# Kernel tuning notes

Measured on AMD Instinct MI355X. Metric: run time of the kernel, lower is better.

The kernel has to match this reference:

```python
import jax, jax.numpy as jnp
import numpy as np

D_MODEL = 1024
N_HEADS = 16
D_K = 64
D_FF = 4096
B = 8
S = 1024
NEG = -1e32
EPS = 1e-5


def _layer_norm(x, g, b):
    mu = jnp.mean(x, axis=-1, keepdims=True)
    var = jnp.var(x, axis=-1, keepdims=True)
    return (x - mu) * jax.lax.rsqrt(var + EPS) * g + b


def setup_inputs() -> dict:
    key = jax.random.key(0)
    ks = jax.random.split(key, 16)
    sc = 0.02
    inp = {
        'x': jax.random.normal(ks[0], (B, S, D_MODEL), dtype=jnp.float32),
        'Wq': jax.random.normal(ks[1], (D_MODEL, D_MODEL), jnp.float32) * sc,
        'bq': jnp.zeros((D_MODEL,), jnp.float32),
        'Wk': jax.random.normal(ks[2], (D_MODEL, D_MODEL), jnp.float32) * sc,
        'bk': jnp.zeros((D_MODEL,), jnp.float32),
        'Wv': jax.random.normal(ks[3], (D_MODEL, D_MODEL), jnp.float32) * sc,
        'bv': jnp.zeros((D_MODEL,), jnp.float32),
        'Wo': jax.random.normal(ks[4], (D_MODEL, D_MODEL), jnp.float32) * sc,
        'bo': jnp.zeros((D_MODEL,), jnp.float32),
        'W1': jax.random.normal(ks[5], (D_MODEL, D_FF), jnp.float32) * sc,
        'b1': jnp.zeros((D_FF,), jnp.float32),
        'W2': jax.random.normal(ks[6], (D_FF, D_MODEL), jnp.float32) * sc,
        'b2': jnp.zeros((D_MODEL,), jnp.float32),
        'g1': jnp.ones((D_MODEL,), jnp.float32),
        'beta1': jnp.zeros((D_MODEL,), jnp.float32),
        'g3': jnp.ones((D_MODEL,), jnp.float32),
        'beta3': jnp.zeros((D_MODEL,), jnp.float32),
    }
    return inp


def _block(x, Wq, bq, Wk, bk, Wv, bv, Wo, bo, W1, b1, W2, b2, g1, beta1, g3, beta3):
    bs, seqlen, _ = x.shape
    # QKV projections -> [b, h, s, d_k]
    def split_heads(t):
        return t.reshape(bs, seqlen, N_HEADS, D_K).transpose(0, 2, 1, 3)
    q = split_heads(x @ Wq + bq)
    k = split_heads(x @ Wk + bk)
    v = split_heads(x @ Wv + bv)
    # scores [b,h,s,s]
    scores = jnp.einsum('bhqd,bhkd->bhqk', q, k) / jnp.sqrt(jnp.float32(D_K))
    # mask=0 case: src_mask = (triu(ones, k=0) == 0) -> allow strictly lower (j < i)
    i = jnp.arange(seqlen)[:, None]
    j = jnp.arange(seqlen)[None, :]
    allowed = (j < i)  # [s, s]
    scores = jnp.where(allowed[None, None], scores, NEG)
    attn = jax.nn.softmax(scores, axis=-1)
    # zero_pad: zero out the first query row of attention probs
    attn = attn * (i > 0).astype(attn.dtype)[None, None]
    ctx = jnp.einsum('bhqk,bhkd->bhqd', attn, v)  # [b,h,s,d_k]
    concat = ctx.transpose(0, 2, 1, 3).reshape(bs, seqlen, D_MODEL)
    attn_out = concat @ Wo + bo
    # residual + LN (dropout p=0)
    h1 = _layer_norm(x + attn_out, g1, beta1)
    # position-wise FFN
    ffn = jax.nn.relu(h1 @ W1 + b1) @ W2 + b2
    out = _layer_norm(h1 + ffn, g3, beta3)
    return out


def reference(x, Wq, bq, Wk, bk, Wv, bv, Wo, bo, W1, b1, W2, b2, g1, beta1, g3, beta3):
    return _block(x, Wq, bq, Wk, bk, Wv, bv, Wo, bo, W1, b1, W2, b2, g1, beta1, g3, beta3)
```

## Files before the change

### kernel.cpp

```cpp
#include <hip/hip_runtime.h>
#include <hip/hip_bf16.h>

typedef __bf16 bf16x8 __attribute__((ext_vector_type(8)));
typedef __bf16 bf16x4 __attribute__((ext_vector_type(4)));
typedef float f32x4 __attribute__((ext_vector_type(4)));
typedef float f32x16 __attribute__((ext_vector_type(16)));

#define GLOBAL_LOAD_LDS16(gp, lp)                                              \
  __builtin_amdgcn_global_load_lds(                                            \
      (const __attribute__((address_space(1))) void*)(gp),                     \
      (__attribute__((address_space(3))) void*)(lp), 16, 0, 0)

__global__ __launch_bounds__(256) void transpose4_f2b_k(
    const float* __restrict__ s0, const float* __restrict__ s1,
    const float* __restrict__ s2, const float* __restrict__ s3,
    __bf16* __restrict__ dst) {
  __shared__ float tile[32][33];
  const float* srcs[4] = {s0, s1, s2, s3};
  const float* src = srcs[blockIdx.z];
  __bf16* d = dst + ((size_t)blockIdx.z << 20);
  const int bx = blockIdx.x * 32, by = blockIdx.y * 32;
  const int tx = threadIdx.x & 31, ty = threadIdx.x >> 5;
#pragma unroll
  for (int i = 0; i < 32; i += 8)
    tile[ty + i][tx] = src[(size_t)(by + ty + i) * 1024 + bx + tx];
  __syncthreads();
#pragma unroll
  for (int i = 0; i < 32; i += 8)
    d[(size_t)(bx + ty + i) * 1024 + by + tx] = (__bf16)tile[tx][ty + i];
}

__global__ __launch_bounds__(256) void transpose_f2b_k(
    const float* __restrict__ src, __bf16* __restrict__ dst, int R, int C) {
  __shared__ float tile[32][33];
  const int bx = blockIdx.x * 32, by = blockIdx.y * 32;
  const int tx = threadIdx.x & 31, ty = threadIdx.x >> 5;
#pragma unroll
  for (int i = 0; i < 32; i += 8)
    tile[ty + i][tx] = src[(size_t)(by + ty + i) * C + bx + tx];
  __syncthreads();
#pragma unroll
  for (int i = 0; i < 32; i += 8)
    dst[(size_t)(bx + ty + i) * R + by + tx] = (__bf16)tile[tx][ty + i];
}

__global__ __launch_bounds__(256) void transpose_v_k(
    const __bf16* __restrict__ src, __bf16* __restrict__ dst) {
  __shared__ __bf16 tile[32][33];
  const int bh = blockIdx.z;
  const int s0 = blockIdx.x * 32, d0 = blockIdx.y * 32;
  const size_t base = (size_t)bh << 16;
  const int tx = threadIdx.x & 31, ty = threadIdx.x >> 5;
#pragma unroll
  for (int i = 0; i < 32; i += 8)
    tile[ty + i][tx] = src[base + (size_t)(s0 + ty + i) * 64 + d0 + tx];
  __syncthreads();
#pragma unroll
  for (int i = 0; i < 32; i += 8)
    dst[base + (size_t)(d0 + ty + i) * 1024 + s0 + tx] = tile[tx][ty + i];
}

__global__ __launch_bounds__(256) void convert_f2b_k(const float* __restrict__ s,
                                                     __bf16* __restrict__ d) {
  const size_t i = ((size_t)blockIdx.x * 256 + threadIdx.x) * 4;
  const float4 v = *(const float4*)(s + i);
  bf16x4 o;
  o[0] = (__bf16)v.x; o[1] = (__bf16)v.y; o[2] = (__bf16)v.z; o[3] = (__bf16)v.w;
  *(bf16x4*)(d + i) = o;
}

__global__ void concat3_k(const float* a, const float* b, const float* c,
                          float* o) {
  int i = blockIdx.x * 256 + threadIdx.x;
  if (i < 1024) o[i] = a[i];
  else if (i < 2048) o[i] = b[i - 1024];
  else if (i < 3072) o[i] = c[i - 2048];
}

template <int EPI>
__global__ __launch_bounds__(256) void gemm_bt32(const __bf16* __restrict__ A,
                                                 const __bf16* __restrict__ Bt,
                                                 const float* __restrict__ bias,
                                                 __bf16* __restrict__ C,
                                                 int M, int N, int K) {
  __shared__ __align__(16) __bf16 As[128 * 64];
  __shared__ __align__(16) __bf16 Bs[128 * 64];
  const int tid = threadIdx.x;
  const int wave = tid >> 6, lane = tid & 63;
  const int l31 = lane & 31, hi = lane >> 5;
  const int wm = wave >> 1, wn = wave & 1;
  const int m0 = blockIdx.x * 128, n0 = blockIdx.y * 128;
  const int srsub = lane >> 3;
  const int sch = lane & 7;

  f32x16 acc[2][2] = {};

  for (int k0 = 0; k0 < K; k0 += 64) {
#pragma unroll
    for (int p = 0; p < 4; ++p) {
      const int g = wave * 4 + p;
      const int row = g * 8 + srsub;
      GLOBAL_LOAD_LDS16(A + (size_t)(m0 + row) * K + k0 + ((sch ^ (row & 7)) * 8),
                        As + g * 512);
      GLOBAL_LOAD_LDS16(Bt + (size_t)(n0 + row) * K + k0 + ((sch ^ (row & 7)) * 8),
                        Bs + g * 512);
    }
    __syncthreads();
#pragma unroll
    for (int kk = 0; kk < 4; ++kk) {
      bf16x8 af[2], bf[2];
#pragma unroll
      for (int mt = 0; mt < 2; ++mt) {
        const int row = wm * 64 + mt * 32 + l31;
        af[mt] = *(const bf16x8*)(As + row * 64 +
                                  (((kk * 2 + hi) ^ (row & 7)) * 8));
      }
#pragma unroll
      for (int nt = 0; nt < 2; ++nt) {
        const int row = wn * 64 + nt * 32 + l31;
        bf[nt] = *(const bf16x8*)(Bs + row * 64 +
                                  (((kk * 2 + hi) ^ (row & 7)) * 8));
      }
#pragma unroll
      for (int mt = 0; mt < 2; ++mt)
#pragma unroll
        for (int nt = 0; nt < 2; ++nt)
          acc[mt][nt] = __builtin_amdgcn_mfma_f32_32x32x16_bf16(
              af[mt], bf[nt], acc[mt][nt], 0, 0, 0);
    }
    __syncthreads();
  }

  float bvv[2];
#pragma unroll
  for (int nt = 0; nt < 2; ++nt) bvv[nt] = bias[n0 + wn * 64 + nt * 32 + l31];
#pragma unroll
  for (int mt = 0; mt < 2; ++mt) {
#pragma unroll
    for (int i = 0; i < 16; ++i) {
      const int row = m0 + wm * 64 + mt * 32 + (i & 3) + 8 * (i >> 2) + 4 * hi;
#pragma unroll
      for (int nt = 0; nt < 2; ++nt) {
        const int col = n0 + wn * 64 + nt * 32 + l31;
        float v = acc[mt][nt][i] + bvv[nt];
        if (EPI == 1) v = fmaxf(v, 0.0f);
        size_t oidx;
        if (EPI == 2) {
          const int which = col >> 10, wi = col & 1023;
          const int h = wi >> 6, d = wi & 63;
          const int b = row >> 10, s = row & 1023;
          oidx = ((size_t)which << 23) +
                 (((size_t)(b * 16 + h) << 16) + s * 64 + d);
        } else {
          oidx = (size_t)row * N + col;
        }
        C[oidx] = (__bf16)v;
      }
    }
  }
}

__global__ __launch_bounds__(256) void gemm_bt64(const __bf16* __restrict__ A,
                                                 const __bf16* __restrict__ Bt,
                                                 const float* __restrict__ bias,
                                                 __bf16* __restrict__ C,
                                                 int M, int N, int K) {
  __shared__ __align__(16) __bf16 As[128 * 64];
  __shared__ __align__(16) __bf16 Bs[64 * 64];
  const int tid = threadIdx.x;
  const int wave = tid >> 6, lane = tid & 63;
  const int quad = lane >> 4, l15 = lane & 15;
  const int wm = wave >> 1, wn = wave & 1;
  const int m0 = blockIdx.x * 128, n0 = blockIdx.y * 64;
  const int srow = tid >> 3;
  const int sch = tid & 7;

  f32x4 acc[4][2] = {};

  for (int k0 = 0; k0 < K; k0 += 64) {
#pragma unroll
    for (int p = 0; p < 4; ++p) {
      const int row = p * 32 + srow;
      GLOBAL_LOAD_LDS16(A + (size_t)(m0 + row) * K + k0 + ((sch ^ (row & 7)) * 8),
                        As + p * 2048 + wave * 512);
    }
#pragma unroll
    for (int p = 0; p < 2; ++p) {
      const int row = p * 32 + srow;
      GLOBAL_LOAD_LDS16(Bt + (size_t)(n0 + row) * K + k0 + ((sch ^ (row & 7)) * 8),
                        Bs + p * 2048 + wave * 512);
    }
    __syncthreads();
    bf16x8 af[4][2], bfr[2][2];
#pragma unroll
    for (int kk = 0; kk < 2; ++kk) {
#pragma unroll
      for (int mt = 0; mt < 4; ++mt) {
        const int row = wm * 64 + mt * 16 + l15;
        af[mt][kk] =
            *(const bf16x8*)(As + row * 64 + (((kk * 4 + quad) ^ (row & 7)) * 8));
      }
#pragma unroll
      for (int nt = 0; nt < 2; ++nt) {
        const int row = wn * 32 + nt * 16 + l15;
        bfr[nt][kk] =
            *(const bf16x8*)(Bs + row * 64 + (((kk * 4 + quad) ^ (row & 7)) * 8));
      }
    }
#pragma unroll
    for (int kk = 0; kk < 2; ++kk)
#pragma unroll
      for (int mt = 0; mt < 4; ++mt)
#pragma unroll
        for (int nt = 0; nt < 2; ++nt)
          acc[mt][nt] = __builtin_amdgcn_mfma_f32_16x16x32_bf16(
              af[mt][kk], bfr[nt][kk], acc[mt][nt], 0, 0, 0);
    __syncthreads();
  }

  float bv[2];
#pragma unroll
  for (int nt = 0; nt < 2; ++nt) bv[nt] = bias[n0 + wn * 32 + nt * 16 + l15];
#pragma unroll
  for (int mt = 0; mt < 4; ++mt) {
#pragma unroll
    for (int r = 0; r < 4; ++r) {
      const int row = m0 + wm * 64 + mt * 16 + quad * 4 + r;
#pragma unroll
      for (int nt = 0; nt < 2; ++nt) {
        const int col = n0 + wn * 32 + nt * 16 + l15;
        C[(size_t)row * N + col] = (__bf16)(acc[mt][nt][r] + bv[nt]);
      }
    }
  }
}

__global__ __launch_bounds__(256) void attn_kernel(const __bf16* __restrict__ Q,
                                                   const __bf16* __restrict__ Kg,
                                                   const __bf16* __restrict__ Vt,
                                                   __bf16* __restrict__ ctx) {
  const int qp = blockIdx.x;
  const int bh = blockIdx.y;
  const int b = bh >> 4, h = bh & 15;
  const int tid = threadIdx.x, wave = tid >> 6, lane = tid & 63;
  const int quad = lane >> 4, l15 = lane & 15;
  const size_t hoff = (size_t)bh << 16;
  const __bf16* Qh = Q + hoff;
  const __bf16* Kh = Kg + hoff;
  const __bf16* Vh = Vt + hoff;

  __shared__ __align__(16) __bf16 Ks[64 * 64];
  __shared__ __align__(16) __bf16 Vs[64 * 64];
  __shared__ __align__(16) __bf16 Ps[4][32 * 72];
  __shared__ float lL[128];

  const int skey = wave * 8 + (lane >> 3);
  const int sgr = lane & 7;

#pragma unroll
  for (int pass = 0; pass < 2; ++pass) {
    const int qt = pass ? (7 - qp) : qp;
    const int qb = qt * 128;

    bf16x8 qf[2][2];
#pragma unroll
    for (int g = 0; g < 2; ++g) {
      const int qrow = qb + wave * 32 + g * 16 + l15;
      bf16x8 t0 = *(const bf16x8*)(Qh + (size_t)qrow * 64 + quad * 8);
      bf16x8 t1 = *(const bf16x8*)(Qh + (size_t)qrow * 64 + 32 + quad * 8);
#pragma unroll
      for (int e = 0; e < 8; ++e) {
        qf[g][0][e] = (__bf16)((float)t0[e] * 0.125f);
        qf[g][1][e] = (__bf16)((float)t1[e] * 0.125f);
      }
    }

    f32x4 oacc[4][2] = {};
    float lrun[2][4] = {};

    const int ktmax = 2 * qt + 1;
    for (int kt = 0; kt <= ktmax; ++kt) {
      __syncthreads();
#pragma unroll
      for (int j = 0; j < 2; ++j) {
        const int row = skey + 32 * j;
        GLOBAL_LOAD_LDS16(
            Kh + (size_t)(kt * 64 + row) * 64 + ((sgr ^ (row & 7)) * 8),
            Ks + j * 2048 + wave * 512);
        GLOBAL_LOAD_LDS16(
            Vh + (size_t)row * 1024 + kt * 64 + ((sgr ^ (row & 7)) * 8),
            Vs + j * 2048 + wave * 512);
      }
      __syncthreads();

      f32x4 sacc[2][4] = {};
#pragma unroll
      for (int nt = 0; nt < 4; ++nt) {
        const int key = nt * 16 + l15, sw = key & 7;
        bf16x8 kf0 = *(const bf16x8*)(Ks + key * 64 + ((quad ^ sw) * 8));
        bf16x8 kf1 = *(const bf16x8*)(Ks + key * 64 + (((quad + 4) ^ sw) * 8));
#pragma unroll
        for (int g = 0; g < 2; ++g) {
          sacc[g][nt] = __builtin_amdgcn_mfma_f32_16x16x32_bf16(
              qf[g][0], kf0, sacc[g][nt], 0, 0, 0);
          sacc[g][nt] = __builtin_amdgcn_mfma_f32_16x16x32_bf16(
              qf[g][1], kf1, sacc[g][nt], 0, 0, 0);
        }
      }

      const bool tilemask = (kt >= 2 * qt);
#pragma unroll
      for (int g = 0; g < 2; ++g)
#pragma unroll
        for (int nt = 0; nt < 4; ++nt) {
          const int key = kt * 64 + nt * 16 + l15;
#pragma unroll
          for (int r = 0; r < 4; ++r) {
            float p = __expf(fminf(sacc[g][nt][r], 60.0f));
            if (tilemask && key >= qb + wave * 32 + g * 16 + quad * 4 + r)
              p = 0.0f;
            sacc[g][nt][r] = p;
            lrun[g][r] += p;
          }
        }

#pragma unroll
      for (int g = 0; g < 2; ++g)
#pragma unroll
        for (int nt = 0; nt < 4; ++nt)
#pragma unroll
          for (int r = 0; r < 4; ++r)
            Ps[wave][(g * 16 + quad * 4 + r) * 72 + nt * 16 + l15] =
                (__bf16)sacc[g][nt][r];

#pragma unroll
      for (int kc = 0; kc < 2; ++kc) {
        bf16x8 pf[2];
#pragma unroll
        for (int g = 0; g < 2; ++g)
          pf[g] = *(const bf16x8*)(&Ps[wave][(g * 16 + l15) * 72 + kc * 32 +
                                             quad * 8]);
#pragma unroll
        for (int mdt = 0; mdt < 4; ++mdt) {
          const int d = mdt * 16 + l15, sw = d & 7;
          bf16x8 vf =
              *(const bf16x8*)(Vs + d * 64 + (((kc * 4 + quad) ^ sw) * 8));
#pragma unroll
          for (int g = 0; g < 2; ++g)
            oacc[mdt][g] = __builtin_amdgcn_mfma_f32_16x16x32_bf16(
                vf, pf[g], oacc[mdt][g], 0, 0, 0);
        }
      }
    }

#pragma unroll
    for (int g = 0; g < 2; ++g)
#pragma unroll
      for (int r = 0; r < 4; ++r) {
        float s = lrun[g][r];
#pragma unroll
        for (int d = 1; d < 16; d <<= 1) s += __shfl_xor(s, d);
        if (l15 == 0) lL[wave * 32 + g * 16 + quad * 4 + r] = s;
      }
    float linv[2];
#pragma unroll
    for (int g = 0; g < 2; ++g) {
      const float l = lL[wave * 32 + g * 16 + l15];
      linv[g] = (qb + wave * 32 + g * 16 + l15 == 0) ? 0.0f : (1.0f / l);
    }
    __bf16* Ot = Ps[wave];
#pragma unroll
    for (int mdt = 0; mdt < 4; ++mdt)
#pragma unroll
      for (int g = 0; g < 2; ++g)
#pragma unroll
        for (int r = 0; r < 4; ++r)
          Ot[(g * 16 + l15) * 72 + mdt * 16 + quad * 4 + r] =
              (__bf16)(oacc[mdt][g][r] * linv[g]);
#pragma unroll
    for (int rr = 0; rr < 2; ++rr)
#pragma unroll
      for (int j = 0; j < 2; ++j) {
        const int row = rr * 16 + (lane >> 2), chk = (lane & 3) + 4 * j;
        bf16x8 ov = *(const bf16x8*)(Ot + row * 72 + chk * 8);
        const size_t oi = ((size_t)(b * 1024 + qb + wave * 32 + row)) * 1024 +
                          h * 64 + chk * 8;
        *(bf16x8*)(ctx + oi) = ov;
      }
  }
}

template <typename TX, typename TY, typename TO>
__global__ __launch_bounds__(256) void add_ln_kernel(const TX* __restrict__ x,
                                                     const TY* __restrict__ y,
                                                     const float* __restrict__ g,
                                                     const float* __restrict__ be,
                                                     TO* __restrict__ out) {
  const int row = blockIdx.x;
  const size_t base = (size_t)row * 1024;
  const int t = threadIdx.x;
  float xv[4], yv[4];
  if constexpr (sizeof(TX) == 4) {
    const float4 a = *(const float4*)(x + base + t * 4);
    xv[0] = a.x; xv[1] = a.y; xv[2] = a.z; xv[3] = a.w;
  } else {
    const bf16x4 a = *(const bf16x4*)(x + base + t * 4);
#pragma unroll
    for (int i = 0; i < 4; ++i) xv[i] = (float)a[i];
  }
  if constexpr (sizeof(TY) == 4) {
    const float4 a = *(const float4*)(y + base + t * 4);
    yv[0] = a.x; yv[1] = a.y; yv[2] = a.z; yv[3] = a.w;
  } else {
    const bf16x4 a = *(const bf16x4*)(y + base + t * 4);
#pragma unroll
    for (int i = 0; i < 4; ++i) yv[i] = (float)a[i];
  }
  float v[4], s = 0.0f, s2 = 0.0f;
#pragma unroll
  for (int i = 0; i < 4; ++i) {
    v[i] = xv[i] + yv[i];
    s += v[i];
    s2 += v[i] * v[i];
  }
#pragma unroll
  for (int m = 1; m < 64; m <<= 1) {
    s += __shfl_xor(s, m);
    s2 += __shfl_xor(s2, m);
  }
  __shared__ float ss[4], ss2[4];
  const int w = t >> 6;
  if ((t & 63) == 0) { ss[w] = s; ss2[w] = s2; }
  __syncthreads();
  s = ss[0] + ss[1] + ss[2] + ss[3];
  s2 = ss2[0] + ss2[1] + ss2[2] + ss2[3];
  const float mu = s * (1.0f / 1024.0f);
  const float var = s2 * (1.0f / 1024.0f) - mu * mu;
  const float rstd = rsqrtf(var + 1e-5f);
#pragma unroll
  for (int i = 0; i < 4; ++i) {
    const float o = (v[i] - mu) * rstd * g[t * 4 + i] + be[t * 4 + i];
    out[base + t * 4 + i] = (TO)o;
  }
}

extern "C" void kernel_launch(void* const* d_in, const int* in_sizes, int n_in,
                              void* d_out, int out_size, void* d_ws,
                              size_t ws_size, hipStream_t stream) {
  (void)in_sizes; (void)n_in; (void)out_size; (void)ws_size;
  const float* x   = (const float*)d_in[0];
  const float* Wq  = (const float*)d_in[1];
  const float* bq  = (const float*)d_in[2];
  const float* Wk  = (const float*)d_in[3];
  const float* bk  = (const float*)d_in[4];
  const float* Wv  = (const float*)d_in[5];
  const float* bv  = (const float*)d_in[6];
  const float* Wo  = (const float*)d_in[7];
  const float* bo  = (const float*)d_in[8];
  const float* W1  = (const float*)d_in[9];
  const float* b1  = (const float*)d_in[10];
  const float* W2  = (const float*)d_in[11];
  const float* b2  = (const float*)d_in[12];
  const float* g1  = (const float*)d_in[13];
  const float* be1 = (const float*)d_in[14];
  const float* g3  = (const float*)d_in[15];
  const float* be3 = (const float*)d_in[16];

  char* ws = (char*)d_ws;
  __bf16* Qb    = (__bf16*)(ws + 0);
  __bf16* Kb    = (__bf16*)(ws + (16u << 20));
  __bf16* Vb    = (__bf16*)(ws + (32u << 20));
  __bf16* ctx   = (__bf16*)(ws + (48u << 20));
  __bf16* mid   = (__bf16*)(ws + 0);
  __bf16* aout  = (__bf16*)(ws + (64u << 20));
  __bf16* h1    = aout;
  __bf16* xb    = (__bf16*)(ws + (80u << 20));
  __bf16* Vtb   = (__bf16*)(ws + (80u << 20));
  __bf16* fout  = (__bf16*)(ws + (80u << 20));
  __bf16* WqkvT = (__bf16*)(ws + (96u << 20));
  __bf16* WoT   = (__bf16*)(ws + (96u << 20) + 3 * (1u << 21));
  __bf16* W1T   = (__bf16*)(ws + (104u << 20));
  __bf16* W2T   = (__bf16*)(ws + (112u << 20));
  float*  bqkv  = (float*)(ws + (120u << 20));
  float*  outp  = (float*)d_out;

  const dim3 blk(256);
  convert_f2b_k<<<dim3(8192), blk, 0, stream>>>(x, xb);
  transpose4_f2b_k<<<dim3(32, 32, 4), blk, 0, stream>>>(Wq, Wk, Wv, Wo, WqkvT);
  transpose_f2b_k<<<dim3(128, 32), blk, 0, stream>>>(W1, W1T, 1024, 4096);
  transpose_f2b_k<<<dim3(32, 128), blk, 0, stream>>>(W2, W2T, 4096, 1024);
  concat3_k<<<dim3(12), blk, 0, stream>>>(bq, bk, bv, bqkv);

  gemm_bt32<2><<<dim3(64, 24), blk, 0, stream>>>(xb, WqkvT, bqkv, Qb, 8192, 3072, 1024);
  transpose_v_k<<<dim3(32, 2, 128), blk, 0, stream>>>(Vb, Vtb);
  attn_kernel<<<dim3(4, 128), blk, 0, stream>>>(Qb, Kb, Vtb, ctx);
  gemm_bt64<<<dim3(64, 16), blk, 0, stream>>>(ctx, WoT, bo, aout, 8192, 1024, 1024);
  add_ln_kernel<float, __bf16, __bf16><<<dim3(8192), blk, 0, stream>>>(
      x, aout, g1, be1, h1);
  gemm_bt32<1><<<dim3(64, 32), blk, 0, stream>>>(h1, W1T, b1, mid, 8192, 4096, 1024);
  gemm_bt64<<<dim3(64, 16), blk, 0, stream>>>(mid, W2T, b2, fout, 8192, 1024, 4096);
  add_ln_kernel<__bf16, __bf16, float><<<dim3(8192), blk, 0, stream>>>(
      h1, fout, g3, be3, outp);
}
```

Before: 482.5 us.

## Replace 128x128 GEMM with double-buffered 256x256 ping-pong GEMM for QKV and FFN1

Swaps the single-buffered 128x128 tile GEMM for a 512-thread, 256x256-tile kernel used by the QKV projection and the first FFN matmul. The new kernel double-buffers the LDS tiles and interleaves global-to-LDS loads with 16x16x32 MFMA phases, using barriers and s_setprio. It also remaps block IDs so that neighbouring tiles spread across the XCDs. The goal is to hide load latency behind compute and raise reuse per tile. The cost is 128KB of LDS per block and fragile hand-placed waitcnt and barrier scheduling.

```diff
diff --git a/kernel.cpp b/kernel.cpp
--- a/kernel.cpp
+++ b/kernel.cpp
@@ -77,87 +77,189 @@
   else if (i < 3072) o[i] = c[i - 2048];
 }
 
+#define STG(P, rowbase, Kld, kbase, DST)                                       \
+  do {                                                                         \
+    GLOBAL_LOAD_LDS16((P) + (size_t)((rowbase) + wave * 16 + srow) * (Kld) +   \
+                          (kbase) + sch8,                                      \
+                      (DST) + wave * 1024);                                    \
+    GLOBAL_LOAD_LDS16((P) + (size_t)((rowbase) + wave * 16 + 8 + srow) *       \
+                              (Kld) + (kbase) + sch8,                          \
+                      (DST) + wave * 1024 + 512);                              \
+  } while (0)
+
+#define LDA(BUF, HALF)                                                         \
+  do {                                                                         \
+    const __bf16* pA_ = &As[BUF][HALF][aoff];                                  \
+    _Pragma("unroll") for (int f_ = 0; f_ < 4; ++f_) {                         \
+      af[f_][0] = *(const bf16x8*)(pA_ + f_ * 1024 + c0);                      \
+      af[f_][1] = *(const bf16x8*)(pA_ + f_ * 1024 + (c0 ^ 32));               \
+    }                                                                          \
+  } while (0)
+
+#define LDB(BUF, CB)                                                           \
+  do {                                                                         \
+    const __bf16* pB_ = &Bs[BUF][CB][boff];                                    \
+    _Pragma("unroll") for (int g_ = 0; g_ < 2; ++g_) {                         \
+      bfr[CB][g_][0] = *(const bf16x8*)(pB_ + g_ * 1024 + c0);                 \
+      bfr[CB][g_][1] = *(const bf16x8*)(pB_ + g_ * 1024 + (c0 ^ 32));          \
+    }                                                                          \
+  } while (0)
+
+#define MFMA16(rb, cb)                                                         \
+  do {                                                                         \
+    _Pragma("unroll") for (int f_ = 0; f_ < 4; ++f_)                           \
+        _Pragma("unroll") for (int g_ = 0; g_ < 2; ++g_) {                     \
+      acc[rb][f_][cb][g_] = __builtin_amdgcn_mfma_f32_16x16x32_bf16(           \
+          af[f_][0], bfr[cb][g_][0], acc[rb][f_][cb][g_], 0, 0, 0);            \
+      acc[rb][f_][cb][g_] = __builtin_amdgcn_mfma_f32_16x16x32_bf16(           \
+          af[f_][1], bfr[cb][g_][1], acc[rb][f_][cb][g_], 0, 0, 0);            \
+    }                                                                          \
+  } while (0)
+
+#define PH_MID()                                                               \
+  do {                                                                         \
+    asm volatile("" ::: "memory");                                             \
+    __builtin_amdgcn_s_barrier();                                              \
+    asm volatile("s_waitcnt lgkmcnt(0)" ::: "memory");                         \
+    __builtin_amdgcn_s_setprio(1);                                             \
+  } while (0)
+
+#define PH_END()                                                               \
+  do {                                                                         \
+    __builtin_amdgcn_s_setprio(0);                                             \
+    asm volatile("" ::: "memory");                                             \
+    __builtin_amdgcn_s_barrier();                                              \
+    asm volatile("" ::: "memory");                                             \
+  } while (0)
+
+#define PH_END_VM(NVM)                                                         \
+  do {                                                                         \
+    __builtin_amdgcn_s_setprio(0);                                             \
+    asm volatile("s_waitcnt vmcnt(" #NVM ")" ::: "memory");                    \
+    __builtin_amdgcn_s_barrier();                                              \
+    asm volatile("" ::: "memory");                                             \
+  } while (0)
+
 template <int EPI>
-__global__ __launch_bounds__(256) void gemm_bt32(const __bf16* __restrict__ A,
-                                                 const __bf16* __restrict__ Bt,
-                                                 const float* __restrict__ bias,
-                                                 __bf16* __restrict__ C,
-                                                 int M, int N, int K) {
-  __shared__ __align__(16) __bf16 As[128 * 64];
-  __shared__ __align__(16) __bf16 Bs[128 * 64];
+__global__ __launch_bounds__(512, 2) void gemm256(const __bf16* __restrict__ A,
+                                                  const __bf16* __restrict__ Bt,
+                                                  const float* __restrict__ bias,
+                                                  __bf16* __restrict__ C,
+                                                  int M, int N, int K) {
+  __shared__ __align__(16) __bf16 As[2][2][128 * 64];
+  __shared__ __align__(16) __bf16 Bs[2][2][128 * 64];
   const int tid = threadIdx.x;
   const int wave = tid >> 6, lane = tid & 63;
-  const int l31 = lane & 31, hi = lane >> 5;
-  const int wm = wave >> 1, wn = wave & 1;
-  const int m0 = blockIdx.x * 128, n0 = blockIdx.y * 128;
-  const int srsub = lane >> 3;
-  const int sch = lane & 7;
-
-  f32x16 acc[2][2] = {};
-
-  for (int k0 = 0; k0 < K; k0 += 64) {
-#pragma unroll
-    for (int p = 0; p < 4; ++p) {
-      const int g = wave * 4 + p;
-      const int row = g * 8 + srsub;
-      GLOBAL_LOAD_LDS16(A + (size_t)(m0 + row) * K + k0 + ((sch ^ (row & 7)) * 8),
-                        As + g * 512);
-      GLOBAL_LOAD_LDS16(Bt + (size_t)(n0 + row) * K + k0 + ((sch ^ (row & 7)) * 8),
-                        Bs + g * 512);
-    }
-    __syncthreads();
-#pragma unroll
-    for (int kk = 0; kk < 4; ++kk) {
-      bf16x8 af[2], bf[2];
-#pragma unroll
-      for (int mt = 0; mt < 2; ++mt) {
-        const int row = wm * 64 + mt * 32 + l31;
-        af[mt] = *(const bf16x8*)(As + row * 64 +
-                                  (((kk * 2 + hi) ^ (row & 7)) * 8));
-      }
-#pragma unroll
-      for (int nt = 0; nt < 2; ++nt) {
-        const int row = wn * 64 + nt * 32 + l31;
-        bf[nt] = *(const bf16x8*)(Bs + row * 64 +
-                                  (((kk * 2 + hi) ^ (row & 7)) * 8));
-      }
-#pragma unroll
-      for (int mt = 0; mt < 2; ++mt)
-#pragma unroll
-        for (int nt = 0; nt < 2; ++nt)
-          acc[mt][nt] = __builtin_amdgcn_mfma_f32_32x32x16_bf16(
-              af[mt], bf[nt], acc[mt][nt], 0, 0, 0);
-    }
-    __syncthreads();
-  }
-
-  float bvv[2];
-#pragma unroll
-  for (int nt = 0; nt < 2; ++nt) bvv[nt] = bias[n0 + wn * 64 + nt * 32 + l31];
-#pragma unroll
-  for (int mt = 0; mt < 2; ++mt) {
-#pragma unroll
-    for (int i = 0; i < 16; ++i) {
-      const int row = m0 + wm * 64 + mt * 32 + (i & 3) + 8 * (i >> 2) + 4 * hi;
-#pragma unroll
-      for (int nt = 0; nt < 2; ++nt) {
-        const int col = n0 + wn * 64 + nt * 32 + l31;
-        float v = acc[mt][nt][i] + bvv[nt];
-        if (EPI == 1) v = fmaxf(v, 0.0f);
-        size_t oidx;
-        if (EPI == 2) {
-          const int which = col >> 10, wi = col & 1023;
-          const int h = wi >> 6, d = wi & 63;
-          const int b = row >> 10, s = row & 1023;
-          oidx = ((size_t)which << 23) +
-                 (((size_t)(b * 16 + h) << 16) + s * 64 + d);
-        } else {
-          oidx = (size_t)row * N + col;
-        }
-        C[oidx] = (__bf16)v;
-      }
-    }
-  }
+  const int quad = lane >> 4, l15 = lane & 15;
+  const int wm = wave >> 2, wn = wave & 3;
+
+  const int nwg = gridDim.x;
+  const int cpx = nwg >> 3;
+  const int bid = blockIdx.x;
+  const int wg = (bid & 7) * cpx + (bid >> 3);
+  const int gy = N >> 8;
+  const int tm = wg / gy, tn = wg - tm * gy;
+  const int m0 = tm << 8, n0 = tn << 8;
+
+  const int srow = lane >> 3;
+  const int sch8 = ((lane & 7) ^ srow) * 8;
+  const int aoff = (wm * 64 + l15) * 64;
+  const int boff = (wn * 32 + l15) * 64;
+  const int c0 = (quad ^ (l15 & 7)) * 8;
+
+  bf16x8 af[4][2], bfr[2][2][2];
+  f32x4 acc[2][4][2][2] = {};
+
+  const int NJ = K >> 7;
+
+  STG(A, m0, K, 0, &As[0][0][0]);
+  STG(Bt, n0, K, 0, &Bs[0][0][0]);
+  STG(A, m0 + 128, K, 0, &As[0][1][0]);
+  STG(Bt, n0 + 128, K, 0, &Bs[0][1][0]);
+  STG(A, m0, K, 64, &As[1][0][0]);
+  STG(Bt, n0, K, 64, &Bs[1][0][0]);
+  asm volatile("s_waitcnt vmcnt(4)" ::: "memory");
+  __builtin_amdgcn_s_barrier();
+  asm volatile("" ::: "memory");
+
+  for (int j = 0; j < NJ; ++j) {
+    const int t1k = (j << 7) + 64, t2k = (j << 7) + 128, t3k = (j << 7) + 192;
+    const bool pf = (j + 1 < NJ);
+    LDA(0, 0);
+    LDB(0, 0);
+    STG(A, m0 + 128, K, t1k, &As[1][1][0]);
+    PH_MID();
+    MFMA16(0, 0);
+    PH_END();
+    LDB(0, 1);
+    STG(Bt, n0 + 128, K, t1k, &Bs[1][1][0]);
+    PH_MID();
+    MFMA16(0, 1);
+    PH_END();
+    LDA(0, 1);
+    if (pf) STG(A, m0, K, t2k, &As[0][0][0]);
+    PH_MID();
+    MFMA16(1, 0);
+    PH_END();
+    if (pf) STG(Bt, n0, K, t2k, &Bs[0][0][0]);
+    PH_MID();
+    MFMA16(1, 1);
+    if (pf) PH_END_VM(4); else PH_END_VM(0);
+    LDA(1, 0);
+    LDB(1, 0);
+    if (pf) STG(A, m0 + 128, K, t2k, &As[0][1][0]);
+    PH_MID();
+    MFMA16(0, 0);
+    PH_END();
+    LDB(1, 1);
+    if (pf) STG(Bt, n0 + 128, K, t2k, &Bs[0][1][0]);
+    PH_MID();
+    MFMA16(0, 1);
+    PH_END();
+    LDA(1, 1);
+    if (pf) STG(A, m0, K, t3k, &As[1][0][0]);
+    PH_MID();
+    MFMA16(1, 0);
+    PH_END();
+    if (pf) STG(Bt, n0, K, t3k, &Bs[1][0][0]);
+    PH_MID();
+    MFMA16(1, 1);
+    if (pf) PH_END_VM(4); else PH_END();
+  }
+
+  float bvv[2][2];
+#pragma unroll
+  for (int cb = 0; cb < 2; ++cb)
+#pragma unroll
+    for (int g = 0; g < 2; ++g)
+      bvv[cb][g] = bias[n0 + cb * 128 + wn * 32 + g * 16 + l15];
+#pragma unroll
+  for (int rb = 0; rb < 2; ++rb)
+#pragma unroll
+    for (int f = 0; f < 4; ++f)
+#pragma unroll
+      for (int i = 0; i < 4; ++i) {
+        const int row = m0 + rb * 128 + wm * 64 + f * 16 + quad * 4 + i;
+#pragma unroll
+        for (int cb = 0; cb < 2; ++cb)
+#pragma unroll
+          for (int g = 0; g < 2; ++g) {
+            const int col = n0 + cb * 128 + wn * 32 + g * 16 + l15;
+            float v = acc[rb][f][cb][g][i] + bvv[cb][g];
+            if (EPI == 1) v = fmaxf(v, 0.0f);
+            size_t oidx;
+            if (EPI == 2) {
+              const int which = col >> 10, wi = col & 1023;
+              const int h = wi >> 6, d = wi & 63;
+              const int b = row >> 10, s = row & 1023;
+              oidx = ((size_t)which << 23) +
+                     (((size_t)(b * 16 + h) << 16) + s * 64 + d);
+            } else {
+              oidx = (size_t)row * N + col;
+            }
+            C[oidx] = (__bf16)v;
+          }
+      }
 }
 
 __global__ __launch_bounds__(256) void gemm_bt64(const __bf16* __restrict__ A,
@@ -485,19 +587,22 @@
   float*  outp  = (float*)d_out;
 
   const dim3 blk(256);
+  const dim3 blk512(512);
   convert_f2b_k<<<dim3(8192), blk, 0, stream>>>(x, xb);
   transpose4_f2b_k<<<dim3(32, 32, 4), blk, 0, stream>>>(Wq, Wk, Wv, Wo, WqkvT);
   transpose_f2b_k<<<dim3(128, 32), blk, 0, stream>>>(W1, W1T, 1024, 4096);
   transpose_f2b_k<<<dim3(32, 128), blk, 0, stream>>>(W2, W2T, 4096, 1024);
   concat3_k<<<dim3(12), blk, 0, stream>>>(bq, bk, bv, bqkv);
 
-  gemm_bt32<2><<<dim3(64, 24), blk, 0, stream>>>(xb, WqkvT, bqkv, Qb, 8192, 3072, 1024);
+  gemm256<2><<<dim3(32 * 12), blk512, 0, stream>>>(xb, WqkvT, bqkv, Qb,
+                                                   8192, 3072, 1024);
   transpose_v_k<<<dim3(32, 2, 128), blk, 0, stream>>>(Vb, Vtb);
   attn_kernel<<<dim3(4, 128), blk, 0, stream>>>(Qb, Kb, Vtb, ctx);
   gemm_bt64<<<dim3(64, 16), blk, 0, stream>>>(ctx, WoT, bo, aout, 8192, 1024, 1024);
   add_ln_kernel<float, __bf16, __bf16><<<dim3(8192), blk, 0, stream>>>(
       x, aout, g1, be1, h1);
-  gemm_bt32<1><<<dim3(64, 32), blk, 0, stream>>>(h1, W1T, b1, mid, 8192, 4096, 1024);
+  gemm256<1><<<dim3(32 * 16), blk512, 0, stream>>>(h1, W1T, b1, mid,
+                                                   8192, 4096, 1024);
   gemm_bt64<<<dim3(64, 16), blk, 0, stream>>>(mid, W2T, b2, fout, 8192, 1024, 4096);
   add_ln_kernel<__bf16, __bf16, float><<<dim3(8192), blk, 0, stream>>>(
       h1, fout, g3, be3, outp);
```

New measurement: 510.0 us. 1.06x slower.

## Replace GEMM kernels with triple-buffered 256x128 tile kernel and XCD-aware block mapping

Applied to the files above, without the earlier changes.

Replaces the two single-buffered GEMM kernels with one templated kernel. It uses 512 threads, a 256x128 output tile and a three-stage LDS ring, issuing global-to-LDS loads two K-tiles ahead. It also adds an XCD-interleaved block-to-tile mapping, raises MFMA priority with s_setprio, and waits on vmcnt before each barrier. The goal is to hide global memory latency and raise MFMA utilization across all four projection GEMMs. In exchange it uses much more LDS and fewer blocks per GEMM, which lowers occupancy and may leave the N=1024 GEMMs with poor wave balance.

```diff
diff --git a/kernel.cpp b/kernel.cpp
--- a/kernel.cpp
+++ b/kernel.cpp
@@ -4,7 +4,6 @@
 typedef __bf16 bf16x8 __attribute__((ext_vector_type(8)));
 typedef __bf16 bf16x4 __attribute__((ext_vector_type(4)));
 typedef float f32x4 __attribute__((ext_vector_type(4)));
-typedef float f32x16 __attribute__((ext_vector_type(16)));
 
 #define GLOBAL_LOAD_LDS16(gp, lp)                                              \
   __builtin_amdgcn_global_load_lds(                                            \
@@ -77,72 +76,119 @@
   else if (i < 3072) o[i] = c[i - 2048];
 }
 
+#define STG(P, rowbase, Kld, kbase, DST)                                       \
+  do {                                                                         \
+    GLOBAL_LOAD_LDS16((P) + (size_t)((rowbase) + wave * 16 + srow) * (Kld) +   \
+                          (kbase) + sch8,                                      \
+                      (DST) + wave * 1024);                                    \
+    GLOBAL_LOAD_LDS16((P) + (size_t)((rowbase) + wave * 16 + 8 + srow) *       \
+                              (Kld) + (kbase) + sch8,                          \
+                      (DST) + wave * 1024 + 512);                              \
+  } while (0)
+
 template <int EPI>
-__global__ __launch_bounds__(256) void gemm_bt32(const __bf16* __restrict__ A,
-                                                 const __bf16* __restrict__ Bt,
-                                                 const float* __restrict__ bias,
-                                                 __bf16* __restrict__ C,
-                                                 int M, int N, int K) {
-  __shared__ __align__(16) __bf16 As[128 * 64];
-  __shared__ __align__(16) __bf16 Bs[128 * 64];
+__global__ __launch_bounds__(512, 2) void gemm_k3(const __bf16* __restrict__ A,
+                                                  const __bf16* __restrict__ Bt,
+                                                  const float* __restrict__ bias,
+                                                  __bf16* __restrict__ C,
+                                                  int M, int N, int K) {
+  __shared__ __align__(16) __bf16 Abuf[3][256 * 64];
+  __shared__ __align__(16) __bf16 Bbuf[3][128 * 64];
   const int tid = threadIdx.x;
   const int wave = tid >> 6, lane = tid & 63;
-  const int l31 = lane & 31, hi = lane >> 5;
+  const int quad = lane >> 4, l15 = lane & 15;
   const int wm = wave >> 1, wn = wave & 1;
-  const int m0 = blockIdx.x * 128, n0 = blockIdx.y * 128;
-  const int srsub = lane >> 3;
-  const int sch = lane & 7;
-
-  f32x16 acc[2][2] = {};
-
-  for (int k0 = 0; k0 < K; k0 += 64) {
-#pragma unroll
-    for (int p = 0; p < 4; ++p) {
-      const int g = wave * 4 + p;
-      const int row = g * 8 + srsub;
-      GLOBAL_LOAD_LDS16(A + (size_t)(m0 + row) * K + k0 + ((sch ^ (row & 7)) * 8),
-                        As + g * 512);
-      GLOBAL_LOAD_LDS16(Bt + (size_t)(n0 + row) * K + k0 + ((sch ^ (row & 7)) * 8),
-                        Bs + g * 512);
-    }
-    __syncthreads();
-#pragma unroll
-    for (int kk = 0; kk < 4; ++kk) {
-      bf16x8 af[2], bf[2];
-#pragma unroll
-      for (int mt = 0; mt < 2; ++mt) {
-        const int row = wm * 64 + mt * 32 + l31;
-        af[mt] = *(const bf16x8*)(As + row * 64 +
-                                  (((kk * 2 + hi) ^ (row & 7)) * 8));
-      }
-#pragma unroll
-      for (int nt = 0; nt < 2; ++nt) {
-        const int row = wn * 64 + nt * 32 + l31;
-        bf[nt] = *(const bf16x8*)(Bs + row * 64 +
-                                  (((kk * 2 + hi) ^ (row & 7)) * 8));
-      }
-#pragma unroll
-      for (int mt = 0; mt < 2; ++mt)
-#pragma unroll
-        for (int nt = 0; nt < 2; ++nt)
-          acc[mt][nt] = __builtin_amdgcn_mfma_f32_32x32x16_bf16(
-              af[mt], bf[nt], acc[mt][nt], 0, 0, 0);
-    }
-    __syncthreads();
-  }
-
-  float bvv[2];
-#pragma unroll
-  for (int nt = 0; nt < 2; ++nt) bvv[nt] = bias[n0 + wn * 64 + nt * 32 + l31];
-#pragma unroll
-  for (int mt = 0; mt < 2; ++mt) {
-#pragma unroll
-    for (int i = 0; i < 16; ++i) {
-      const int row = m0 + wm * 64 + mt * 32 + (i & 3) + 8 * (i >> 2) + 4 * hi;
-#pragma unroll
-      for (int nt = 0; nt < 2; ++nt) {
-        const int col = n0 + wn * 64 + nt * 32 + l31;
-        float v = acc[mt][nt][i] + bvv[nt];
+
+  const int nwg = gridDim.x;
+  const int cpx = nwg >> 3;
+  const int bid = blockIdx.x;
+  const int wg = (bid & 7) * cpx + (bid >> 3);
+  const int gy = N >> 7;
+  const int tm = wg / gy, tn = wg - tm * gy;
+  const int m0 = tm << 8, n0 = tn << 7;
+
+  const int srow = lane >> 3;
+  const int sch8 = ((lane & 7) ^ srow) * 8;
+  const int aoff = (wm * 64 + l15) * 64;
+  const int boff = (wn * 64 + l15) * 64;
+  const int c0 = (quad ^ (l15 & 7)) * 8;
+
+  bf16x8 af[4][2], bfr[4][2];
+  f32x4 acc[4][4] = {};
+
+  const int NT = K >> 6;
+
+  const __bf16* a_c = Abuf[0];
+  const __bf16* a_n = Abuf[1];
+  const __bf16* a_f = Abuf[2];
+  const __bf16* b_c = Bbuf[0];
+  const __bf16* b_n = Bbuf[1];
+  const __bf16* b_f = Bbuf[2];
+
+  STG(A, m0, K, 0, (__bf16*)a_c);
+  STG(A, m0 + 128, K, 0, (__bf16*)a_c + 128 * 64);
+  STG(Bt, n0, K, 0, (__bf16*)b_c);
+  STG(A, m0, K, 64, (__bf16*)a_n);
+  STG(A, m0 + 128, K, 64, (__bf16*)a_n + 128 * 64);
+  STG(Bt, n0, K, 64, (__bf16*)b_n);
+  asm volatile("s_waitcnt vmcnt(6)" ::: "memory");
+  __builtin_amdgcn_s_barrier();
+  asm volatile("" ::: "memory");
+
+  for (int t = 0; t < NT; ++t) {
+#pragma unroll
+    for (int f = 0; f < 4; ++f) {
+      af[f][0] = *(const bf16x8*)(a_c + aoff + f * 1024 + c0);
+      af[f][1] = *(const bf16x8*)(a_c + aoff + f * 1024 + (c0 ^ 32));
+    }
+#pragma unroll
+    for (int g = 0; g < 4; ++g) {
+      bfr[g][0] = *(const bf16x8*)(b_c + boff + g * 1024 + c0);
+      bfr[g][1] = *(const bf16x8*)(b_c + boff + g * 1024 + (c0 ^ 32));
+    }
+    const int kf = (t + 2) << 6;
+    const bool pf = (t + 2 < NT);
+    if (pf) {
+      STG(A, m0, K, kf, (__bf16*)a_f);
+      STG(A, m0 + 128, K, kf, (__bf16*)a_f + 128 * 64);
+      STG(Bt, n0, K, kf, (__bf16*)b_f);
+    }
+    __builtin_amdgcn_s_setprio(1);
+#pragma unroll
+    for (int f = 0; f < 4; ++f)
+#pragma unroll
+      for (int g = 0; g < 4; ++g) {
+        acc[f][g] = __builtin_amdgcn_mfma_f32_16x16x32_bf16(
+            af[f][0], bfr[g][0], acc[f][g], 0, 0, 0);
+        acc[f][g] = __builtin_amdgcn_mfma_f32_16x16x32_bf16(
+            af[f][1], bfr[g][1], acc[f][g], 0, 0, 0);
+      }
+    __builtin_amdgcn_s_setprio(0);
+    if (pf) {
+      asm volatile("s_waitcnt vmcnt(6)" ::: "memory");
+      __builtin_amdgcn_s_barrier();
+      asm volatile("" ::: "memory");
+    } else if (t + 1 < NT) {
+      asm volatile("s_waitcnt vmcnt(0)" ::: "memory");
+      __builtin_amdgcn_s_barrier();
+      asm volatile("" ::: "memory");
+    }
+    const __bf16* ta = a_c; a_c = a_n; a_n = a_f; a_f = ta;
+    const __bf16* tb = b_c; b_c = b_n; b_n = b_f; b_f = tb;
+  }
+
+  float bvv[4];
+#pragma unroll
+  for (int g = 0; g < 4; ++g) bvv[g] = bias[n0 + wn * 64 + g * 16 + l15];
+#pragma unroll
+  for (int f = 0; f < 4; ++f)
+#pragma unroll
+    for (int i = 0; i < 4; ++i) {
+      const int row = m0 + wm * 64 + f * 16 + quad * 4 + i;
+#pragma unroll
+      for (int g = 0; g < 4; ++g) {
+        const int col = n0 + wn * 64 + g * 16 + l15;
+        float v = acc[f][g][i] + bvv[g];
         if (EPI == 1) v = fmaxf(v, 0.0f);
         size_t oidx;
         if (EPI == 2) {
@@ -157,82 +203,6 @@
         C[oidx] = (__bf16)v;
       }
     }
-  }
-}
-
-__global__ __launch_bounds__(256) void gemm_bt64(const __bf16* __restrict__ A,
-                                                 const __bf16* __restrict__ Bt,
-                                                 const float* __restrict__ bias,
-                                                 __bf16* __restrict__ C,
-                                                 int M, int N, int K) {
-  __shared__ __align__(16) __bf16 As[128 * 64];
-  __shared__ __align__(16) __bf16 Bs[64 * 64];
-  const int tid = threadIdx.x;
-  const int wave = tid >> 6, lane = tid & 63;
-  const int quad = lane >> 4, l15 = lane & 15;
-  const int wm = wave >> 1, wn = wave & 1;
-  const int m0 = blockIdx.x * 128, n0 = blockIdx.y * 64;
-  const int srow = tid >> 3;
-  const int sch = tid & 7;
-
-  f32x4 acc[4][2] = {};
-
-  for (int k0 = 0; k0 < K; k0 += 64) {
-#pragma unroll
-    for (int p = 0; p < 4; ++p) {
-      const int row = p * 32 + srow;
-      GLOBAL_LOAD_LDS16(A + (size_t)(m0 + row) * K + k0 + ((sch ^ (row & 7)) * 8),
-                        As + p * 2048 + wave * 512);
-    }
-#pragma unroll
-    for (int p = 0; p < 2; ++p) {
-      const int row = p * 32 + srow;
-      GLOBAL_LOAD_LDS16(Bt + (size_t)(n0 + row) * K + k0 + ((sch ^ (row & 7)) * 8),
-                        Bs + p * 2048 + wave * 512);
-    }
-    __syncthreads();
-    bf16x8 af[4][2], bfr[2][2];
-#pragma unroll
-    for (int kk = 0; kk < 2; ++kk) {
-#pragma unroll
-      for (int mt = 0; mt < 4; ++mt) {
-        const int row = wm * 64 + mt * 16 + l15;
-        af[mt][kk] =
-            *(const bf16x8*)(As + row * 64 + (((kk * 4 + quad) ^ (row & 7)) * 8));
-      }
-#pragma unroll
-      for (int nt = 0; nt < 2; ++nt) {
-        const int row = wn * 32 + nt * 16 + l15;
-        bfr[nt][kk] =
-            *(const bf16x8*)(Bs + row * 64 + (((kk * 4 + quad) ^ (row & 7)) * 8));
-      }
-    }
-#pragma unroll
-    for (int kk = 0; kk < 2; ++kk)
-#pragma unroll
-      for (int mt = 0; mt < 4; ++mt)
-#pragma unroll
-        for (int nt = 0; nt < 2; ++nt)
-          acc[mt][nt] = __builtin_amdgcn_mfma_f32_16x16x32_bf16(
-              af[mt][kk], bfr[nt][kk], acc[mt][nt], 0, 0, 0);
-    __syncthreads();
-  }
-
-  float bv[2];
-#pragma unroll
-  for (int nt = 0; nt < 2; ++nt) bv[nt] = bias[n0 + wn * 32 + nt * 16 + l15];
-#pragma unroll
-  for (int mt = 0; mt < 4; ++mt) {
-#pragma unroll
-    for (int r = 0; r < 4; ++r) {
-      const int row = m0 + wm * 64 + mt * 16 + quad * 4 + r;
-#pragma unroll
-      for (int nt = 0; nt < 2; ++nt) {
-        const int col = n0 + wn * 32 + nt * 16 + l15;
-        C[(size_t)row * N + col] = (__bf16)(acc[mt][nt][r] + bv[nt]);
-      }
-    }
-  }
 }
 
 __global__ __launch_bounds__(256) void attn_kernel(const __bf16* __restrict__ Q,
@@ -485,20 +455,25 @@
   float*  outp  = (float*)d_out;
 
   const dim3 blk(256);
+  const dim3 blk512(512);
   convert_f2b_k<<<dim3(8192), blk, 0, stream>>>(x, xb);
   transpose4_f2b_k<<<dim3(32, 32, 4), blk, 0, stream>>>(Wq, Wk, Wv, Wo, WqkvT);
   transpose_f2b_k<<<dim3(128, 32), blk, 0, stream>>>(W1, W1T, 1024, 4096);
   transpose_f2b_k<<<dim3(32, 128), blk, 0, stream>>>(W2, W2T, 4096, 1024);
   concat3_k<<<dim3(12), blk, 0, stream>>>(bq, bk, bv, bqkv);
 
-  gemm_bt32<2><<<dim3(64, 24), blk, 0, stream>>>(xb, WqkvT, bqkv, Qb, 8192, 3072, 1024);
+  gemm_k3<2><<<dim3(32 * 24), blk512, 0, stream>>>(xb, WqkvT, bqkv, Qb,
+                                                   8192, 3072, 1024);
   transpose_v_k<<<dim3(32, 2, 128), blk, 0, stream>>>(Vb, Vtb);
   attn_kernel<<<dim3(4, 128), blk, 0, stream>>>(Qb, Kb, Vtb, ctx);
-  gemm_bt64<<<dim3(64, 16), blk, 0, stream>>>(ctx, WoT, bo, aout, 8192, 1024, 1024);
+  gemm_k3<0><<<dim3(32 * 8), blk512, 0, stream>>>(ctx, WoT, bo, aout,
+                                                  8192, 1024, 1024);
   add_ln_kernel<float, __bf16, __bf16><<<dim3(8192), blk, 0, stream>>>(
       x, aout, g1, be1, h1);
-  gemm_bt32<1><<<dim3(64, 32), blk, 0, stream>>>(h1, W1T, b1, mid, 8192, 4096, 1024);
-  gemm_bt64<<<dim3(64, 16), blk, 0, stream>>>(mid, W2T, b2, fout, 8192, 1024, 4096);
+  gemm_k3<1><<<dim3(32 * 32), blk512, 0, stream>>>(h1, W1T, b1, mid,
+                                                   8192, 4096, 1024);
+  gemm_k3<0><<<dim3(32 * 8), blk512, 0, stream>>>(mid, W2T, b2, fout,
+                                                  8192, 1024, 4096);
   add_ln_kernel<__bf16, __bf16, float><<<dim3(8192), blk, 0, stream>>>(
       h1, fout, g3, be3, outp);
 }
```

Measured after the change: 471.2 us. 1.02x faster.
